# Kernel tuning notes

Hardware: AMD Instinct MI355X
Metric: run time of the kernel (lower is better)

## Reference

```python
import jax, jax.numpy as jnp
import numpy as np

GAMMA = 1.0
INF_REPLACE = 1e10  # original code replaces inf with 1e10 before logsumexp


def _softmin3(r_diag, r_up, r_left, gamma):
    # softmin over the 3 DP neighbors (stack order matches original: diag, up, left)
    x = jnp.stack([r_diag, r_up, r_left], axis=0)  # (3, B)
    x = jnp.where(jnp.isinf(x), jnp.asarray(INF_REPLACE, x.dtype), x)
    return -gamma * jax.nn.logsumexp(-x / gamma, axis=0)  # (B,)


def _cdist(X, Y):
    # Euclidean pairwise distance, torch.cdist(p=2): (B,N,d),(B,M,d) -> (B,N,M)
    d2 = (jnp.sum(X * X, axis=-1)[:, :, None]
          + jnp.sum(Y * Y, axis=-1)[:, None, :]
          - 2.0 * jnp.einsum('bnd,bmd->bnm', X, Y))
    return jnp.sqrt(jnp.maximum(d2, 0.0))


def _soft_dtw(X, Y, gamma):
    B, N, _ = X.shape
    D = _cdist(X, Y)  # (B, N, N)
    inf = jnp.asarray(jnp.inf, D.dtype)

    # R row 0: [0, inf, inf, ...] per batch
    prev_row0 = jnp.full((B, N + 1), inf, dtype=D.dtype).at[:, 0].set(0.0)

    def row_step(prev_row, d_row):
        # prev_row: (B, N+1) = R[i-1, :]; d_row: (B, N) = D[:, i-1, :]
        xs = (d_row.T, prev_row[:, :-1].T, prev_row[:, 1:].T)  # each (N, B)

        def col_step(r_left, x):
            d, r_diag, r_up = x  # each (B,)
            r = d + _softmin3(r_diag, r_up, r_left, gamma)
            return r, r

        _, row = jax.lax.scan(col_step, jnp.full((B,), inf, dtype=D.dtype), xs)
        new_row = jnp.concatenate([jnp.full((B, 1), inf, dtype=D.dtype), row.T], axis=1)
        return new_row, None

    last_row, _ = jax.lax.scan(row_step, prev_row0, jnp.swapaxes(D, 0, 1))
    return last_row[:, -1]  # R[:, N, N], shape (B,)


def setup_inputs() -> dict:
    key = jax.random.key(0)
    kx, ky = jax.random.split(key)
    B, N, d = 64, 512, 64
    X = jax.random.normal(kx, (B, N, d), dtype=jnp.float32)
    Y = jax.random.normal(ky, (B, N, d), dtype=jnp.float32)
    return {"X": X, "Y": Y}


def reference(X, Y):
    return _soft_dtw(X, Y, GAMMA)
```

## Files before the change

kernel.cpp:

```cpp
#include <hip/hip_runtime.h>
#include <math.h>

#define NB 64
#define NN 512
#define ND 64

#define LOG2E 1.4426950408889634f
#define LN2   0.6931471805599453f
#define RING  16
#define SD    592
#define NINF  __int_as_float(0xFF800000u)

typedef __attribute__((ext_vector_type(8))) short  bf16x8;
typedef __attribute__((ext_vector_type(4))) float  f32x4;

static __device__ __forceinline__ unsigned short f2bf(float f) {
    unsigned u = __float_as_uint(f);
    u += 0x7FFFu + ((u >> 16) & 1u);
    return (unsigned short)(u >> 16);
}

__global__ __launch_bounds__(256) void pack_kernel(const float* __restrict__ X,
                                                   const float* __restrict__ Y,
                                                   unsigned short* __restrict__ Xp,
                                                   unsigned short* __restrict__ Yp,
                                                   float* __restrict__ nx,
                                                   float* __restrict__ ny) {
    const int gid = blockIdx.x * 256 + threadIdx.x;
    const float* src;
    unsigned short* dst;
    float* ndst;
    if (blockIdx.y == 0) { src = X + (size_t)gid * ND; dst = Xp; ndst = nx; }
    else                 { src = Y + (size_t)gid * ND; dst = Yp; ndst = ny; }

    float v[ND];
    float s = 0.f;
    #pragma unroll
    for (int k = 0; k < ND; k += 4) {
        float4 f = *(const float4*)(src + k);
        v[k] = f.x; v[k + 1] = f.y; v[k + 2] = f.z; v[k + 3] = f.w;
        s += f.x * f.x + f.y * f.y + f.z * f.z + f.w * f.w;
    }
    ndst[gid] = s;

    const int b  = gid >> 9;
    const int i  = gid & 511;
    const int it = i >> 4;
    const int lm = i & 15;
    #pragma unroll
    for (int h = 0; h < 2; ++h) {
        #pragma unroll
        for (int q = 0; q < 4; ++q) {
            unsigned w[4];
            #pragma unroll
            for (int m = 0; m < 4; ++m) {
                const int c = h * 32 + q * 8 + 2 * m;
                w[m] = (unsigned)f2bf(v[c]) | ((unsigned)f2bf(v[c + 1]) << 16);
            }
            uint4 pkt; pkt.x = w[0]; pkt.y = w[1]; pkt.z = w[2]; pkt.w = w[3];
            *(uint4*)(dst + ((((size_t)b * 32 + it) * 2 + h) << 9)
                          + (size_t)(q * 16 + lm) * 8) = pkt;
        }
    }
}

__global__ __launch_bounds__(256) void cdist_kernel(const unsigned short* __restrict__ Xp,
                                                    const unsigned short* __restrict__ Yp,
                                                    const float* __restrict__ nx,
                                                    const float* __restrict__ ny,
                                                    uint2* __restrict__ Wd) {
    const int b  = blockIdx.z;
    const int ib = blockIdx.x * 128;
    const int jb = blockIdx.y * 128;
    const int t  = threadIdx.x;

    const int wave = t >> 6;
    const int wi   = (wave & 1) * 64;
    const int wj   = (wave >> 1) * 64;
    const int lane = t & 63;
    const int lm   = lane & 15;
    const int quad = lane >> 4;

    f32x4 acc[4][4];
    #pragma unroll
    for (int mt = 0; mt < 4; ++mt)
        #pragma unroll
        for (int nt = 0; nt < 4; ++nt)
            acc[mt][nt] = (f32x4){0.f, 0.f, 0.f, 0.f};

    const int jt0 = (jb + wj) >> 4;
    const int it0 = (ib + wi) >> 4;

    #pragma unroll
    for (int h = 0; h < 2; ++h) {
        bf16x8 Af[4], Bf[4];
        #pragma unroll
        for (int mt = 0; mt < 4; ++mt)
            Af[mt] = *(const bf16x8*)(Yp
                + ((((size_t)b * 32 + jt0 + mt) * 2 + h) << 9) + (size_t)lane * 8);
        #pragma unroll
        for (int nt = 0; nt < 4; ++nt)
            Bf[nt] = *(const bf16x8*)(Xp
                + ((((size_t)b * 32 + it0 + nt) * 2 + h) << 9) + (size_t)lane * 8);
        #pragma unroll
        for (int mt = 0; mt < 4; ++mt)
            #pragma unroll
            for (int nt = 0; nt < 4; ++nt)
                acc[mt][nt] = __builtin_amdgcn_mfma_f32_16x16x32_bf16(
                    Af[mt], Bf[nt], acc[mt][nt], 0, 0, 0);
    }

    float nxv[4];
    float4 nyv[4];
    #pragma unroll
    for (int nt = 0; nt < 4; ++nt)
        nxv[nt] = nx[(size_t)b * NN + ib + wi + nt * 16 + lm];
    #pragma unroll
    for (int mt = 0; mt < 4; ++mt)
        nyv[mt] = *(const float4*)(ny + (size_t)b * NN + jb + wj + mt * 16 + quad * 4);

    #pragma unroll
    for (int nt = 0; nt < 4; ++nt) {
        const int i = ib + wi + nt * 16 + lm;
        #pragma unroll
        for (int mt = 0; mt < 4; ++mt) {
            const int j0 = jb + wj + mt * 16 + quad * 4;
            const int wv = j0 >> 8;
            const int tt = (j0 >> 2) & 63;
            const float* nyp = (const float*)&nyv[mt];
            unsigned a[4];
            #pragma unroll
            for (int r = 0; r < 4; ++r) {
                float d2 = nyp[r] + nxv[nt] - 2.0f * acc[mt][nt][r];
                float w  = __builtin_amdgcn_exp2f(16.0f - LOG2E * sqrtf(fmaxf(d2, 0.f)));
                a[r] = __float_as_uint(w) + 0x8000u;
            }
            uint2 pkt;
            pkt.x = (a[0] >> 16) | (a[1] & 0xFFFF0000u);
            pkt.y = (a[2] >> 16) | (a[3] & 0xFFFF0000u);
            Wd[((size_t)(b * 2 + wv) * SD + (size_t)(i + tt)) * 64 + tt] = pkt;
        }
    }
}

static __device__ __forceinline__ float dpp_shr1(float x, float old) {
    return __int_as_float(__builtin_amdgcn_update_dpp(
        __float_as_int(old), __float_as_int(x), 0x138, 0xf, 0xf, false));
}
static __device__ __forceinline__ float dpp_shl1(float x) {
    return __int_as_float(__builtin_amdgcn_update_dpp(
        0, __float_as_int(x), 0x130, 0xf, 0xf, false));
}

static __device__ __forceinline__ void dtw_step4(
    bool W1, bool DOACT, bool DOGUARD, bool DOREN,
    int ss, int u, int t, const uint2* __restrict__ Wdw,
    uint2* ring, float* L, float& diagHold, float& h, float& Otf,
    float& hbuf, float* __restrict__ h0)
{
    float recvH = dpp_shr1(h, NINF);
    if (W1) {
        recvH = (t == 0) ? hbuf : recvH;
        hbuf  = dpp_shl1(hbuf);
    }
    if (DOACT) { if (ss == t && (t > 0 || W1)) Otf = -recvH; }

    const float up0   = __builtin_amdgcn_exp2f(fminf(recvH + Otf, 80.0f));
    const float diag0 = diagHold;
    diagHold = up0 * 65536.0f;

    const int j = ss - t + 1;
    const uint2 c = ring[u];

    ring[u] = Wdw[(size_t)(ss + RING) * 64];

    bool act = true;
    if (DOGUARD) act = (j >= 1) && (j <= NN);
    if (act) {
        float dd[4];
        dd[0] = __uint_as_float(c.x << 16);
        dd[1] = __uint_as_float(c.x & 0xFFFF0000u);
        dd[2] = __uint_as_float(c.y << 16);
        dd[3] = __uint_as_float(c.y & 0xFFFF0000u);

        float pre[4], cc[4];
        pre[0] = diag0 + L[0];
        #pragma unroll
        for (int k = 1; k < 4; ++k)
            pre[k] = fmaf(65536.0f, L[k - 1], L[k]);
        #pragma unroll
        for (int k = 0; k < 4; ++k) cc[k] = dd[k] * pre[k];
        float r = up0;
        #pragma unroll
        for (int k = 0; k < 4; ++k) {
            r = fmaf(dd[k], r, cc[k]);
            L[k] = r;
        }

        if (DOREN) {
            float m4 = fmaxf(fmaxf(L[0], L[1]), fmaxf(L[2], L[3]));
            const int   e  = (int)(__float_as_uint(m4) >> 23) - 127;
            const float sc = __uint_as_float((unsigned)(127 - e) << 23);
            #pragma unroll
            for (int k = 0; k < 4; ++k) L[k] *= sc;
            diagHold *= sc;
            Otf -= (float)e;
        }

        h = __builtin_amdgcn_logf(L[3]) - Otf;
        if (!W1) h0[j] = h;
    }
}

static __device__ __forceinline__ void run_chunk(
    bool W1, bool ACT, bool GUARD, int base,
    int t, const uint2* __restrict__ Wdw,
    uint2* ring, float* L, float& diagHold, float& h, float& Otf,
    float& hbuf, float* __restrict__ h0)
{
    for (int sb = 0; sb < 64; sb += RING)
        #pragma unroll
        for (int u = 0; u < RING; ++u)
            dtw_step4(W1, ACT, GUARD, (u & 1) == 1,
                      base + sb + u, u, t, Wdw, ring, L,
                      diagHold, h, Otf, hbuf, h0);
}

__global__ __launch_bounds__(128) void dtw_kernel(const uint2* __restrict__ Wd,
                                                  float* __restrict__ out) {
    __shared__ float h0[584];
    const int b    = blockIdx.x;
    const int tid  = threadIdx.x;
    const int t    = tid & 63;
    const int wave = tid >> 6;
    const uint2* __restrict__ Wdw = Wd + ((size_t)(b * 2 + wave) * SD) * 64 + t;

    float L[4] = {0.f, 0.f, 0.f, 0.f};
    float diagHold = (wave == 0 && t == 0) ? 65536.0f : 0.0f;
    float h = NINF, Otf = 0.0f, hbuf = NINF;

    uint2 ring[RING];
    #pragma unroll
    for (int u = 0; u < RING; ++u)
        ring[u] = Wdw[(size_t)u * 64];

    for (int wall = 0; wall < 11; ++wall) {
        const int ch = wave ? wall - 2 : wall;
        if (wave == 0) {
            if (ch == 0)
                run_chunk(false, true,  true,  0,      t, Wdw, ring, L, diagHold, h, Otf, hbuf, h0);
            else if (ch >= 1 && ch <= 7)
                run_chunk(false, false, false, ch*64,  t, Wdw, ring, L, diagHold, h, Otf, hbuf, h0);
            else if (ch == 8)
                run_chunk(false, false, true,  512,    t, Wdw, ring, L, diagHold, h, Otf, hbuf, h0);
        } else {
            if (ch == 0)
                run_chunk(true,  true,  true,  0,      t, Wdw, ring, L, diagHold, h, Otf, hbuf, h0);
            else if (ch >= 1 && ch <= 7)
                run_chunk(true,  false, false, ch*64,  t, Wdw, ring, L, diagHold, h, Otf, hbuf, h0);
            else if (ch == 8)
                run_chunk(true,  false, true,  512,    t, Wdw, ring, L, diagHold, h, Otf, hbuf, h0);
        }
        __syncthreads();
        if (wave && wall >= 1 && wall <= 9)
            hbuf = h0[(wall - 1) * 64 + 1 + t];
    }

    if (wave == 1 && t == 63) out[b] = (16384.0f - h) * LN2;
}

extern "C" void kernel_launch(void* const* d_in, const int* in_sizes, int n_in,
                              void* d_out, int out_size, void* d_ws, size_t ws_size,
                              hipStream_t stream) {
    const float* X = (const float*)d_in[0];
    const float* Y = (const float*)d_in[1];
    float* out = (float*)d_out;

    char* ws = (char*)d_ws;
    uint2* Wd = (uint2*)ws;
    unsigned short* Xp = (unsigned short*)(ws + 41943040);
    unsigned short* Yp = (unsigned short*)(ws + 41943040 + 4194304);
    float* nx = (float*)(ws + 41943040 + 2 * 4194304);
    float* ny = (float*)(ws + 41943040 + 2 * 4194304 + 131072);

    pack_kernel<<<dim3(NB * NN / 256, 2), 256, 0, stream>>>(X, Y, Xp, Yp, nx, ny);
    cdist_kernel<<<dim3(4, 4, NB), 256, 0, stream>>>(Xp, Yp, nx, ny, Wd);
    dtw_kernel<<<NB, 128, 0, stream>>>(Wd, out);
}
```

Before: 143.4 us.

## Stage DTW distance stream through LDS with dedicated producer waves

Adds two producer waves per block that copy the skewed distance rows from global memory into a 128-row LDS ring, 32 rows ahead of the compute waves. The two compute waves then fill their register prefetch ring from LDS instead of global memory, and the ring shrinks from 16 to 8. The wavefront chunks are halved to 32 steps, so there are twice as many block barriers. The goal is to hide global load latency from the serial recurrence, at the cost of more synchronisation and about 128KB of LDS per block.

Measured after the change: 191.5 us. +33.5%, slower.

```diff
diff --git a/kernel.cpp b/kernel.cpp
--- a/kernel.cpp
+++ b/kernel.cpp
@@ -7,7 +7,7 @@
 
 #define LOG2E 1.4426950408889634f
 #define LN2   0.6931471805599453f
-#define RING  16
+#define RING  8
 #define SD    592
 #define NINF  __int_as_float(0xFF800000u)
 
@@ -154,7 +154,7 @@
 
 static __device__ __forceinline__ void dtw_step4(
     bool W1, bool DOACT, bool DOGUARD, bool DOREN,
-    int ss, int u, int t, const uint2* __restrict__ Wdw,
+    int ss, int u, int t, const uint2 (* __restrict__ P)[64],
     uint2* ring, float* L, float& diagHold, float& h, float& Otf,
     float& hbuf, float* __restrict__ h0)
 {
@@ -172,7 +172,7 @@
     const int j = ss - t + 1;
     const uint2 c = ring[u];
 
-    ring[u] = Wdw[(size_t)(ss + RING) * 64];
+    ring[u] = P[(ss + RING) & 127][t];
 
     bool act = true;
     if (DOGUARD) act = (j >= 1) && (j <= NN);
@@ -214,56 +214,86 @@
 
 static __device__ __forceinline__ void run_chunk(
     bool W1, bool ACT, bool GUARD, int base,
-    int t, const uint2* __restrict__ Wdw,
+    int t, const uint2 (* __restrict__ P)[64],
     uint2* ring, float* L, float& diagHold, float& h, float& Otf,
     float& hbuf, float* __restrict__ h0)
 {
-    for (int sb = 0; sb < 64; sb += RING)
+    for (int sb = 0; sb < 32; sb += RING)
         #pragma unroll
         for (int u = 0; u < RING; ++u)
             dtw_step4(W1, ACT, GUARD, (u & 1) == 1,
-                      base + sb + u, u, t, Wdw, ring, L,
+                      base + sb + u, u, t, P, ring, L,
                       diagHold, h, Otf, hbuf, h0);
 }
 
-__global__ __launch_bounds__(128) void dtw_kernel(const uint2* __restrict__ Wd,
+__global__ __launch_bounds__(256) void dtw_kernel(const uint2* __restrict__ Wd,
                                                   float* __restrict__ out) {
+    __shared__ __align__(16) uint2 lring[2][128][64];
     __shared__ float h0[584];
     const int b    = blockIdx.x;
     const int tid  = threadIdx.x;
     const int t    = tid & 63;
     const int wave = tid >> 6;
-    const uint2* __restrict__ Wdw = Wd + ((size_t)(b * 2 + wave) * SD) * 64 + t;
+
+    const int lp = (wave >= 2) ? (wave - 2) : 0;
+    const uint4* __restrict__ gp =
+        (const uint4*)(Wd + ((size_t)(b * 2 + lp) * SD) * 64);
+
+    if (wave >= 2) {
+        uint4* l4 = (uint4*)&lring[lp][0][0];
+        #pragma unroll
+        for (int k = 0; k < 32; ++k)
+            l4[t + 64 * k] = gp[t + 64 * k];
+    }
 
     float L[4] = {0.f, 0.f, 0.f, 0.f};
     float diagHold = (wave == 0 && t == 0) ? 65536.0f : 0.0f;
     float h = NINF, Otf = 0.0f, hbuf = NINF;
-
     uint2 ring[RING];
-    #pragma unroll
-    for (int u = 0; u < RING; ++u)
-        ring[u] = Wdw[(size_t)u * 64];
-
-    for (int wall = 0; wall < 11; ++wall) {
-        const int ch = wave ? wall - 2 : wall;
+    const uint2 (* __restrict__ P)[64] = lring[wave & 1];
+
+    __syncthreads();
+
+    if (wave < 2) {
+        #pragma unroll
+        for (int u = 0; u < RING; ++u)
+            ring[u] = P[u][t];
+    }
+
+    for (int w = 0; w < 22; ++w) {
         if (wave == 0) {
-            if (ch == 0)
-                run_chunk(false, true,  true,  0,      t, Wdw, ring, L, diagHold, h, Otf, hbuf, h0);
-            else if (ch >= 1 && ch <= 7)
-                run_chunk(false, false, false, ch*64,  t, Wdw, ring, L, diagHold, h, Otf, hbuf, h0);
-            else if (ch == 8)
-                run_chunk(false, false, true,  512,    t, Wdw, ring, L, diagHold, h, Otf, hbuf, h0);
+            if (w <= 1)
+                run_chunk(false, true,  true,  32*w, t, P, ring, L, diagHold, h, Otf, hbuf, h0);
+            else if (w <= 15)
+                run_chunk(false, false, false, 32*w, t, P, ring, L, diagHold, h, Otf, hbuf, h0);
+            else if (w <= 17)
+                run_chunk(false, false, true,  32*w, t, P, ring, L, diagHold, h, Otf, hbuf, h0);
+        } else if (wave == 1) {
+            const int c2 = w - 4;
+            if (c2 >= 0) {
+                if (c2 <= 1)
+                    run_chunk(true, true,  true,  32*c2, t, P, ring, L, diagHold, h, Otf, hbuf, h0);
+                else if (c2 <= 15)
+                    run_chunk(true, false, false, 32*c2, t, P, ring, L, diagHold, h, Otf, hbuf, h0);
+                else
+                    run_chunk(true, false, true,  32*c2, t, P, ring, L, diagHold, h, Otf, hbuf, h0);
+            }
         } else {
-            if (ch == 0)
-                run_chunk(true,  true,  true,  0,      t, Wdw, ring, L, diagHold, h, Otf, hbuf, h0);
-            else if (ch >= 1 && ch <= 7)
-                run_chunk(true,  false, false, ch*64,  t, Wdw, ring, L, diagHold, h, Otf, hbuf, h0);
-            else if (ch == 8)
-                run_chunk(true,  false, true,  512,    t, Wdw, ring, L, diagHold, h, Otf, hbuf, h0);
+            const int  s0 = (lp == 0) ? 32 * (w + 2) : 32 * (w - 2);
+            const bool on = (lp == 0) ? (w <= 16) : (w >= 4 && w <= 20);
+            if (on) {
+                int nrows = 592 - s0; if (nrows > 32) nrows = 32;
+                const uint4* gs = gp + (size_t)s0 * 32;
+                uint4* ls = (uint4*)&lring[lp][s0 & 127][0];
+                const int kn = nrows >> 1;
+                #pragma unroll
+                for (int k = 0; k < 16; ++k)
+                    if (k < kn) ls[t + 64 * k] = gs[t + 64 * k];
+            }
         }
         __syncthreads();
-        if (wave && wall >= 1 && wall <= 9)
-            hbuf = h0[(wall - 1) * 64 + 1 + t];
+        if (wave == 1 && (w & 1) && w >= 3 && w <= 19)
+            hbuf = h0[(w - 3) * 32 + 1 + t];
     }
 
     if (wave == 1 && t == 63) out[b] = (16384.0f - h) * LN2;
@@ -285,5 +315,5 @@
 
     pack_kernel<<<dim3(NB * NN / 256, 2), 256, 0, stream>>>(X, Y, Xp, Yp, nx, ny);
     cdist_kernel<<<dim3(4, 4, NB), 256, 0, stream>>>(Xp, Yp, nx, ny, Wd);
-    dtw_kernel<<<NB, 128, 0, stream>>>(Wd, out);
-}
+    dtw_kernel<<<NB, 256, 0, stream>>>(Wd, out);
+}
```
